# Performance work log

Measured on AMD Instinct MI355X. Metric: run time of the kernel, lower is better.

The kernel has to match this reference:

```python
import jax, jax.numpy as jnp
import numpy as np

B, L, LC, C, CTX, H = 4, 2048, 512, 1024, 1024, 16
D = C // H
EPS = 1e-6
SCALE = 1.0 / np.float32(np.sqrt(D))


def _ln(x):
    # LayerNorm32, elementwise_affine applied outside when present
    mu = jnp.mean(x, axis=-1, keepdims=True)
    var = jnp.var(x, axis=-1, keepdims=True)
    return (x - mu) * jax.lax.rsqrt(var + EPS)


def _attn(q, k, v):
    # q: [B,Lq,H,D], k/v: [B,Lk,H,D] -> [B,Lq,C]
    s = jnp.einsum('bqhd,bkhd->bhqk', q, k) * SCALE
    p = jax.nn.softmax(s, axis=-1)
    o = jnp.einsum('bhqk,bkhd->bqhd', p, v)
    return o.reshape(o.shape[0], o.shape[1], C)


def setup_inputs() -> dict:
    key = jax.random.key(0)
    ks = jax.random.split(key, 12)
    s = 0.02
    w = lambda k, shape: (jax.random.normal(k, shape, jnp.float32) * s)
    z = lambda n: jnp.zeros((n,), jnp.float32)
    return {
        'x': jax.random.normal(ks[0], (B, L, C), jnp.float32),
        'mod': jax.random.normal(ks[1], (B, C), jnp.float32),
        'context': jax.random.normal(ks[2], (B, LC, CTX), jnp.float32),
        'w_ada': w(ks[3], (C, 6 * C)), 'b_ada': z(6 * C),
        'w_qkv': w(ks[4], (C, 3 * C)), 'b_qkv': z(3 * C),
        'w_so': w(ks[5], (C, C)), 'b_so': z(C),
        'g_n2': jnp.ones((C,), jnp.float32), 'b_n2': z(C),
        'w_cq': w(ks[6], (C, C)), 'b_cq': z(C),
        'w_ckv': w(ks[7], (CTX, 2 * C)), 'b_ckv': z(2 * C),
        'w_co': w(ks[8], (C, C)), 'b_co': z(C),
        'w_m1': w(ks[9], (C, 4 * C)), 'b_m1': z(4 * C),
        'w_m2': w(ks[10], (4 * C, C)), 'b_m2': z(C),
    }


def reference(x, mod, context, w_ada, b_ada, w_qkv, b_qkv, w_so, b_so,
              g_n2, b_n2, w_cq, b_cq, w_ckv, b_ckv, w_co, b_co,
              w_m1, b_m1, w_m2, b_m2):
    # adaLN modulation: SiLU -> Linear(C, 6C) -> chunk(6)
    ada = jax.nn.silu(mod) @ w_ada + b_ada  # [B, 6C]
    sh_msa, sc_msa, g_msa, sh_mlp, sc_mlp, g_mlp = jnp.split(ada, 6, axis=-1)
    ex = lambda t: t[:, None, :]  # broadcast per-sample over its token run

    # --- MSA branch ---
    h = _ln(x) * (1.0 + ex(sc_msa)) + ex(sh_msa)
    qkv = (h @ w_qkv + b_qkv).reshape(B, L, 3, H, D)
    h = _attn(qkv[:, :, 0], qkv[:, :, 1], qkv[:, :, 2]) @ w_so + b_so
    x = x + h * ex(g_msa)

    # --- MCA branch (norm2 has affine) ---
    h = _ln(x) * g_n2 + b_n2
    q = (h @ w_cq + b_cq).reshape(B, L, H, D)
    kv = (context @ w_ckv + b_ckv).reshape(B, LC, 2, H, D)
    h = _attn(q, kv[:, :, 0], kv[:, :, 1]) @ w_co + b_co
    x = x + h

    # --- FFN branch ---
    h = _ln(x) * (1.0 + ex(sc_mlp)) + ex(sh_mlp)
    h = jax.nn.gelu(h @ w_m1 + b_m1, approximate=False) @ w_m2 + b_m2
    x = x + h * ex(g_mlp)
    return x
```

## Files before the change

### kernel.cpp

```cpp
#include <hip/hip_runtime.h>
#include <cstdint>

typedef __bf16 bf16;
typedef __bf16 bf16x8 __attribute__((ext_vector_type(8)));
typedef __bf16 bf16x4 __attribute__((ext_vector_type(4)));
typedef float  floatx4 __attribute__((ext_vector_type(4)));
typedef unsigned int uint32x4 __attribute__((ext_vector_type(4)));

#define B_  4
#define L_  2048
#define LC_ 512
#define C_  1024
#define H_  16
#define D_  64

typedef const __attribute__((address_space(1))) unsigned int* as1_u32p;
typedef __attribute__((address_space(3))) unsigned int* as3_u32p;

__device__ __forceinline__ void async16(const void* g, void* l) {
  __builtin_amdgcn_global_load_lds((as1_u32p)g, (as3_u32p)l, 16, 0, 0);
}

__device__ __forceinline__ floatx4 mfma16(bf16x8 a, bf16x8 b, floatx4 c) {
  return __builtin_amdgcn_mfma_f32_16x16x32_bf16(a, b, c, 0, 0, 0);
}

__device__ __forceinline__ bool dt_bf16(const unsigned* dt) { return dt[0] == 0x3F803F80u; }

__device__ __forceinline__ float rd(const void* p, size_t i, bool bf) {
  return bf ? (float)((const bf16*)p)[i] : ((const float*)p)[i];
}

__global__ __launch_bounds__(256) void k_cvt(const void* __restrict__ src, bf16* __restrict__ dst,
                                             int N, const unsigned* __restrict__ dt) {
  bool bf = dt_bf16(dt);
  int i = (blockIdx.x * 256 + threadIdx.x) * 4;
  if (i + 3 < N) {
    for (int j = 0; j < 4; ++j) dst[i + j] = (bf16)rd(src, i + j, bf);
  } else {
    for (int j = 0; j < 4 && i + j < N; ++j) dst[i + j] = (bf16)rd(src, i + j, bf);
  }
}

struct CvtSrcs { const void* s[9]; };
__global__ __launch_bounds__(256) void k_cvt_all(CvtSrcs c, bf16* __restrict__ dst,
                                                 const unsigned* __restrict__ dt) {
  bool bf = dt_bf16(dt);
  int i = blockIdx.x * 256 + threadIdx.x;
  if (i >= 15360) return;
  const int pre[10] = {0, 3072, 4096, 5120, 6144, 7168, 9216, 10240, 14336, 15360};
  int seg = 0;
  #pragma unroll
  for (int k = 1; k < 9; ++k) if (i >= pre[k]) seg = k;
  dst[i] = (bf16)rd(c.s[seg], i - pre[seg], bf);
}

__global__ __launch_bounds__(256) void k_silu(const void* __restrict__ mod, float* __restrict__ sm,
                                              const unsigned* __restrict__ dt) {
  bool bf = dt_bf16(dt);
  int i = blockIdx.x * 256 + threadIdx.x;
  if (i < B_ * C_) {
    float v = rd(mod, i, bf);
    sm[i] = v / (1.f + __expf(-v));
  }
}

__global__ __launch_bounds__(256) void k_ada(const float* __restrict__ sm, const void* __restrict__ w,
                                             float* __restrict__ part, const unsigned* __restrict__ dt) {
  bool bf = dt_bf16(dt);
  int idx = blockIdx.x * 256 + threadIdx.x;
  int b = idx / 6144, j = idx - b * 6144;
  int k0 = blockIdx.y * 256;
  const float* s = sm + b * C_;
  float acc = 0.f;
  if (bf) {
    const bf16* W = (const bf16*)w;
    for (int k = k0; k < k0 + 256; ++k) acc += s[k] * (float)W[(size_t)k * 6144 + j];
  } else {
    const float* W = (const float*)w;
    for (int k = k0; k < k0 + 256; ++k) acc += s[k] * W[(size_t)k * 6144 + j];
  }
  part[(size_t)blockIdx.y * 24576 + idx] = acc;
}

__global__ __launch_bounds__(256) void k_ada_red(const float* __restrict__ part, const void* __restrict__ bv,
                                                 float* __restrict__ ada, const unsigned* __restrict__ dt) {
  bool bf = dt_bf16(dt);
  int idx = blockIdx.x * 256 + threadIdx.x;
  int j = idx % 6144;
  ada[idx] = rd(bv, j, bf) + part[idx] + part[24576 + idx] + part[49152 + idx] + part[73728 + idx];
}

struct TransDesc { const void* src; bf16* dst; int R, Cc, nCb, pre; };
struct TransDescs { TransDesc d[7]; };
__global__ __launch_bounds__(256) void k_trans_all(TransDescs t, const unsigned* __restrict__ dt) {
  bool bf = dt_bf16(dt);
  __shared__ bf16 tile[32][33];
  int blk = blockIdx.x;
  int di = 0;
  #pragma unroll
  for (int i = 1; i < 7; ++i) if (blk >= t.d[i].pre) di = i;
  const void* src = t.d[di].src;
  bf16* dst = t.d[di].dst;
  int R = t.d[di].R, Cc = t.d[di].Cc;
  int local = blk - t.d[di].pre;
  int bx = local % t.d[di].nCb, by = local / t.d[di].nCb;
  int c0 = bx * 32, r0 = by * 32;
  int tx = threadIdx.x & 31, ty = threadIdx.x >> 5;
  for (int i = 0; i < 4; ++i)
    tile[ty * 4 + i][tx] = (bf16)rd(src, (size_t)(r0 + ty * 4 + i) * Cc + c0 + tx, bf);
  __syncthreads();
  for (int i = 0; i < 4; ++i)
    dst[(size_t)(c0 + ty * 4 + i) * R + r0 + tx] = tile[tx][ty * 4 + i];
}

__global__ __launch_bounds__(256) void k_vt(const bf16* __restrict__ src, int ld, int off, int Lk,
                                            bf16* __restrict__ VT) {
  __shared__ bf16 tile[32][33];
  int l0 = blockIdx.x * 32;
  int d0 = blockIdx.y * 32;
  int bh = blockIdx.z, b = bh >> 4, h = bh & 15;
  int tx = threadIdx.x & 31, ty = threadIdx.x >> 5;
  for (int i = 0; i < 4; ++i) {
    int l = l0 + ty * 4 + i;
    tile[ty * 4 + i][tx] = src[((size_t)b * Lk + l) * ld + off + h * 64 + d0 + tx];
  }
  __syncthreads();
  for (int i = 0; i < 4; ++i) {
    int d = d0 + ty * 4 + i;
    VT[((size_t)bh * 64 + d) * Lk + l0 + tx] = tile[tx][ty * 4 + i];
  }
}

__global__ __launch_bounds__(256) void k_ln(const void* __restrict__ xraw, const float* __restrict__ xf,
                                            const unsigned* __restrict__ dt, bf16* __restrict__ out,
                                            const float* __restrict__ ada, int scOff, int shOff, float scAdd,
                                            const bf16* __restrict__ gcol, const bf16* __restrict__ bcol) {
  int row = blockIdx.x;
  int b = row >> 11;
  int base = row * C_ + threadIdx.x * 4;
  float v[4];
  if (xf) {
    for (int i = 0; i < 4; ++i) v[i] = xf[base + i];
  } else {
    bool bf = dt_bf16(dt);
    for (int i = 0; i < 4; ++i) v[i] = rd(xraw, base + i, bf);
  }
  float s1 = 0.f, s2 = 0.f;
  for (int i = 0; i < 4; ++i) { s1 += v[i]; s2 += v[i] * v[i]; }
  for (int m = 1; m < 64; m <<= 1) { s1 += __shfl_xor(s1, m); s2 += __shfl_xor(s2, m); }
  __shared__ float r1[4], r2[4];
  int w = threadIdx.x >> 6;
  if ((threadIdx.x & 63) == 0) { r1[w] = s1; r2[w] = s2; }
  __syncthreads();
  s1 = r1[0] + r1[1] + r1[2] + r1[3];
  s2 = r2[0] + r2[1] + r2[2] + r2[3];
  float mu = s1 * (1.f / (float)C_);
  float var = fmaxf(s2 * (1.f / (float)C_) - mu * mu, 0.f);
  float rstd = rsqrtf(var + 1e-6f);
  for (int i = 0; i < 4; ++i) {
    int c = threadIdx.x * 4 + i;
    float sc, sh;
    if (ada) { sc = scAdd + ada[b * 6144 + scOff + c]; sh = ada[b * 6144 + shOff + c]; }
    else     { sc = (float)gcol[c];                    sh = (float)bcol[c]; }
    out[base + i] = (bf16)((v[i] - mu) * rstd * sc + sh);
  }
}

template <int MODE>
__global__ __launch_bounds__(256) void k_gemm(const bf16* __restrict__ A, const bf16* __restrict__ Bt,
                                              const bf16* __restrict__ bias, void* __restrict__ outv,
                                              int M, int N, int K,
                                              const void* __restrict__ resid,
                                              const float* __restrict__ ada, int gateOff,
                                              const unsigned* __restrict__ dt,
                                              float qs, int qN) {
  __shared__ bf16 As[2 * 8192];
  __shared__ bf16 Bs[2 * 8192];
  const int tid = threadIdx.x;
  const int w = tid >> 6, lane = tid & 63;
  const int wr = w & 1, wc = w >> 1;
  const int g = lane >> 4, t = lane & 15;

  const int nbx = gridDim.x;
  const int nwg = nbx * gridDim.y;
  const int orig = blockIdx.y * nbx + blockIdx.x;
  const int qq = nwg >> 3, rrm = nwg & 7;
  const int xcd = orig & 7, sidx = orig >> 3;
  const int wgid = (xcd < rrm ? xcd * (qq + 1) : rrm * (qq + 1) + (xcd - rrm) * qq) + sidx;
  const int rowA0 = (wgid / nbx) * 128, rowB0 = (wgid % nbx) * 128;

  const int scol = ((lane & 3) ^ ((lane >> 3) & 3)) * 8;
  const bf16* Ag = A  + (size_t)(rowA0 + w * 32 + (lane >> 2)) * K + scol;
  const bf16* Bg = Bt + (size_t)(rowB0 + w * 32 + (lane >> 2)) * K + scol;

  auto stage = [&](int kb, int bufsel) {
    bf16* Ad = As + bufsel * 8192 + w * 1024;
    bf16* Bd = Bs + bufsel * 8192 + w * 1024;
    async16(Ag + kb,                       Ad);
    async16(Ag + kb + (size_t)16 * K,      Ad + 512);
    async16(Ag + kb + 32,                  Ad + 4096);
    async16(Ag + kb + 32 + (size_t)16 * K, Ad + 4096 + 512);
    async16(Bg + kb,                       Bd);
    async16(Bg + kb + (size_t)16 * K,      Bd + 512);
    async16(Bg + kb + 32,                  Bd + 4096);
    async16(Bg + kb + 32 + (size_t)16 * K, Bd + 4096 + 512);
  };

  floatx4 acc[4][4];
  for (int i = 0; i < 4; ++i) for (int j = 0; j < 4; ++j) for (int r = 0; r < 4; ++r) acc[i][j][r] = 0.f;

  stage(0, 0);
  __syncthreads();

  const int rsw = (t >> 1) & 3;

  const int nkb = K >> 6;
  for (int it = 0; it < nkb; ++it) {
    const int cur = it & 1;
    if (it + 1 < nkb) stage((it + 1) << 6, cur ^ 1);
    const bf16* Asb = As + cur * 8192;
    const bf16* Bsb = Bs + cur * 8192;
    __builtin_amdgcn_s_setprio(1);
    #pragma unroll
    for (int kk = 0; kk < 2; ++kk) {
      const int gc = (g ^ rsw) * 8;
      bf16x8 af[4], bfr[4];
      #pragma unroll
      for (int mt = 0; mt < 4; ++mt) af[mt]  = *(const bf16x8*)&Asb[kk * 4096 + (wr * 64 + mt * 16 + t) * 32 + gc];
      #pragma unroll
      for (int nt = 0; nt < 4; ++nt) bfr[nt] = *(const bf16x8*)&Bsb[kk * 4096 + (wc * 64 + nt * 16 + t) * 32 + gc];
      #pragma unroll
      for (int mt = 0; mt < 4; ++mt)
        #pragma unroll
        for (int nt = 0; nt < 4; ++nt)
          acc[mt][nt] = mfma16(af[mt], bfr[nt], acc[mt][nt]);
    }
    __builtin_amdgcn_s_setprio(0);
    if (it + 1 < nkb) __syncthreads();
  }

  const bool bf = (MODE == 1 || MODE == 4) ? dt_bf16(dt) : false;
  for (int mt = 0; mt < 4; ++mt) {
    for (int nt = 0; nt < 4; ++nt) {
      int grow = rowA0 + wr * 64 + mt * 16 + g * 4;
      int gcol = rowB0 + wc * 64 + nt * 16 + t;
      float bvv = (float)bias[gcol];
      for (int r = 0; r < 4; ++r) {
        int rr = grow + r;
        float v = acc[mt][nt][r] + bvv;
        size_t idx = (size_t)rr * N + gcol;
        if (MODE == 0) {
          ((bf16*)outv)[idx] = (bf16)(v * ((gcol < qN) ? qs : 1.0f));
        } else if (MODE == 1) {
          float gt = ada[(rr >> 11) * 6144 + gateOff + gcol];
          ((float*)outv)[idx] = rd(resid, idx, bf) + v * gt;
        } else if (MODE == 2) {
          ((float*)outv)[idx] = ((const float*)resid)[idx] + v;
        } else if (MODE == 3) {
          ((bf16*)outv)[idx] = (bf16)(0.5f * v * (1.f + erff(v * 0.70710678118654752f)));
        } else {
          float gt = ada[(rr >> 11) * 6144 + gateOff + gcol];
          float val = ((const float*)resid)[idx] + v * gt;
          if (bf) ((bf16*)outv)[idx] = (bf16)val;
          else    ((float*)outv)[idx] = val;
        }
      }
    }
  }
}

template <int MODE>
__global__ __launch_bounds__(512) void k_gemm8(const bf16* __restrict__ A, const bf16* __restrict__ Bt,
                                               const bf16* __restrict__ bias, void* __restrict__ outv,
                                               int M, int N, int K,
                                               const void* __restrict__ resid,
                                               const float* __restrict__ ada, int gateOff,
                                               const unsigned* __restrict__ dt,
                                               float qs, int qN) {
  __shared__ bf16 As[2 * 16384];
  __shared__ bf16 Bs[2 * 16384];
  const int tid = threadIdx.x;
  const int lane = tid & 63;
  const int wid = tid >> 6;
  const int wrw = wid & 1, wcw = wid >> 1;
  const int g = lane >> 4, t = lane & 15;

  const int nbx = gridDim.x;
  const int nwg = nbx * gridDim.y;
  const int orig = blockIdx.y * nbx + blockIdx.x;
  const int qq = nwg >> 3, rrm = nwg & 7;
  const int xcd = orig & 7, sidx = orig >> 3;
  const int wgid = (xcd < rrm ? xcd * (qq + 1) : rrm * (qq + 1) + (xcd - rrm) * qq) + sidx;
  const int rowA0 = (wgid / nbx) * 256, rowB0 = (wgid % nbx) * 256;

  const int srow = tid >> 3;
  const int sch = ((tid & 7) ^ (srow & 7)) * 8;
  const bf16* Ag = A  + (size_t)(rowA0 + srow) * K + sch;
  const bf16* Bg = Bt + (size_t)(rowB0 + srow) * K + sch;
  const size_t rstep = (size_t)64 * K;

  floatx4 acc[8][4];
  #pragma unroll
  for (int i = 0; i < 8; ++i)
    #pragma unroll
    for (int j = 0; j < 4; ++j)
      for (int r = 0; r < 4; ++r) acc[i][j][r] = 0.f;

  const int nkb = K >> 6;
  #pragma unroll
  for (int j = 0; j < 4; ++j) async16(Ag + (size_t)j * rstep, As + j * 4096 + tid * 8);
  #pragma unroll
  for (int j = 0; j < 4; ++j) async16(Bg + (size_t)j * rstep, Bs + j * 4096 + tid * 8);

  const int t7 = t & 7;

  for (int T = 0; T < nkb; ++T) {
    const int cur = T & 1;
    const bool st = (T + 1 < nkb);
    const int kb1 = (T + 1) << 6;
    bf16* Asn = As + (cur ^ 1) * 16384;
    bf16* Bsn = Bs + (cur ^ 1) * 16384;

    if (st) {
      async16(Ag + kb1,         Asn + tid * 8);
      async16(Ag + rstep + kb1, Asn + 4096 + tid * 8);
      asm volatile("s_waitcnt vmcnt(2)" ::: "memory");
    } else {
      asm volatile("s_waitcnt vmcnt(0)" ::: "memory");
    }
    __builtin_amdgcn_s_barrier();

    const bf16* Ac = As + cur * 16384;
    const bf16* Bc = Bs + cur * 16384;

    bf16x8 bfr[4];
    #pragma unroll
    for (int nf = 0; nf < 4; ++nf)
      bfr[nf] = *(const bf16x8*)&Bc[(wcw * 64 + nf * 16 + t) * 64 + ((0 * 4 + g) ^ t7) * 8];
    {
      bf16x8 af[4];
      #pragma unroll
      for (int mf = 0; mf < 4; ++mf)
        af[mf] = *(const bf16x8*)&Ac[(wrw * 128 + mf * 16 + t) * 64 + ((0 * 4 + g) ^ t7) * 8];
      __builtin_amdgcn_s_setprio(1);
      #pragma unroll
      for (int mf = 0; mf < 4; ++mf)
        #pragma unroll
        for (int nf = 0; nf < 4; ++nf)
          acc[mf][nf] = mfma16(af[mf], bfr[nf], acc[mf][nf]);
      __builtin_amdgcn_s_setprio(0);
    }
    if (st) {
      async16(Ag + 2 * rstep + kb1, Asn + 2 * 4096 + tid * 8);
      async16(Ag + 3 * rstep + kb1, Asn + 3 * 4096 + tid * 8);
    }
    {
      bf16x8 af[4];
      #pragma unroll
      for (int mf = 0; mf < 4; ++mf)
        af[mf] = *(const bf16x8*)&Ac[(wrw * 128 + (mf + 4) * 16 + t) * 64 + ((0 * 4 + g) ^ t7) * 8];
      __builtin_amdgcn_s_setprio(1);
      #pragma unroll
      for (int mf = 0; mf < 4; ++mf)
        #pragma unroll
        for (int nf = 0; nf < 4; ++nf)
          acc[mf + 4][nf] = mfma16(af[mf], bfr[nf], acc[mf + 4][nf]);
      __builtin_amdgcn_s_setprio(0);
    }
    if (st) {
      async16(Bg + kb1,         Bsn + tid * 8);
      async16(Bg + rstep + kb1, Bsn + 4096 + tid * 8);
    }
    #pragma unroll
    for (int nf = 0; nf < 4; ++nf)
      bfr[nf] = *(const bf16x8*)&Bc[(wcw * 64 + nf * 16 + t) * 64 + ((1 * 4 + g) ^ t7) * 8];
    {
      bf16x8 af[4];
      #pragma unroll
      for (int mf = 0; mf < 4; ++mf)
        af[mf] = *(const bf16x8*)&Ac[(wrw * 128 + mf * 16 + t) * 64 + ((1 * 4 + g) ^ t7) * 8];
      __builtin_amdgcn_s_setprio(1);
      #pragma unroll
      for (int mf = 0; mf < 4; ++mf)
        #pragma unroll
        for (int nf = 0; nf < 4; ++nf)
          acc[mf][nf] = mfma16(af[mf], bfr[nf], acc[mf][nf]);
      __builtin_amdgcn_s_setprio(0);
    }
    if (st) {
      async16(Bg + 2 * rstep + kb1, Bsn + 2 * 4096 + tid * 8);
      async16(Bg + 3 * rstep + kb1, Bsn + 3 * 4096 + tid * 8);
    }
    {
      bf16x8 af[4];
      #pragma unroll
      for (int mf = 0; mf < 4; ++mf)
        af[mf] = *(const bf16x8*)&Ac[(wrw * 128 + (mf + 4) * 16 + t) * 64 + ((1 * 4 + g) ^ t7) * 8];
      __builtin_amdgcn_s_setprio(1);
      #pragma unroll
      for (int mf = 0; mf < 4; ++mf)
        #pragma unroll
        for (int nf = 0; nf < 4; ++nf)
          acc[mf + 4][nf] = mfma16(af[mf], bfr[nf], acc[mf + 4][nf]);
      __builtin_amdgcn_s_setprio(0);
    }
    asm volatile("s_waitcnt lgkmcnt(0)" ::: "memory");
    __builtin_amdgcn_s_barrier();
  }

  const bool bf = (MODE == 1 || MODE == 4) ? dt_bf16(dt) : false;
  #pragma unroll
  for (int mf = 0; mf < 8; ++mf) {
    #pragma unroll
    for (int nf = 0; nf < 4; ++nf) {
      int grow = rowA0 + wrw * 128 + mf * 16 + g * 4;
      int gcol = rowB0 + wcw * 64 + nf * 16 + t;
      float bvv = (float)bias[gcol];
      for (int r = 0; r < 4; ++r) {
        int rr = grow + r;
        float v = acc[mf][nf][r] + bvv;
        size_t idx = (size_t)rr * N + gcol;
        if (MODE == 0) {
          ((bf16*)outv)[idx] = (bf16)(v * ((gcol < qN) ? qs : 1.0f));
        } else if (MODE == 1) {
          float gt = ada[(rr >> 11) * 6144 + gateOff + gcol];
          ((float*)outv)[idx] = rd(resid, idx, bf) + v * gt;
        } else if (MODE == 2) {
          ((float*)outv)[idx] = ((const float*)resid)[idx] + v;
        } else if (MODE == 3) {
          ((bf16*)outv)[idx] = (bf16)(0.5f * v * (1.f + erff(v * 0.70710678118654752f)));
        } else {
          float gt = ada[(rr >> 11) * 6144 + gateOff + gcol];
          float val = ((const float*)resid)[idx] + v * gt;
          if (bf) ((bf16*)outv)[idx] = (bf16)val;
          else    ((float*)outv)[idx] = val;
        }
      }
    }
  }
}

__global__ __launch_bounds__(512) void k_attn(const bf16* __restrict__ Qb, int ldq, int qoff,
                                              const bf16* __restrict__ Kb, int ldk, int koff,
                                              const bf16* __restrict__ VT,
                                              bf16* __restrict__ Ob, int Lk) {
  __shared__ bf16 smem[24576];

  const int tid = threadIdx.x;
  const int w = tid >> 6, lane = tid & 63;
  const int g = lane >> 4, t = lane & 15;
  const int bh = blockIdx.y, b = bh >> 4, h = bh & 15;
  const int q0 = blockIdx.x * 128;

  const bf16* Q  = Qb + (size_t)(b * L_ + q0) * ldq + h * 64 + qoff;
  const bf16* K  = Kb + (size_t)b * Lk * ldk + h * 64 + koff;
  const bf16* Vt = VT + (size_t)bh * 64 * Lk;
  const int rowQ = w * 16 + t;
  bf16* O = Ob + ((size_t)(b * L_ + q0 + rowQ)) * C_ + h * 64;

  const int sp  = lane & 7;
  const int sq0 = w * 16 + (lane >> 3);
  const int sq1 = sq0 + 8;
  const int swq0 = (sp ^ (sq0 & 7)) * 8;
  const int swq1 = (sp ^ (sq1 & 7)) * 8;
  const int skr = w * 8 + (lane >> 3);
  const int swk = (sp ^ (skr & 7)) * 8;

  bf16* Ps  = smem;
  bf16* KB0 = smem + 8192;
  bf16* VB0 = smem + 16384;

  async16(Q + (size_t)sq0 * ldq + swq0, smem + w * 1024);
  async16(Q + (size_t)sq1 * ldq + swq1, smem + w * 1024 + 512);
  async16(K + (size_t)skr * ldk + swk, KB0 + w * 512);
  async16(Vt + (size_t)skr * Lk + swk, VB0 + w * 512);
  __syncthreads();

  bf16x8 bq[2];
  #pragma unroll
  for (int ko = 0; ko < 2; ++ko)
    bq[ko] = *(const bf16x8*)&smem[rowQ * 64 + (((ko * 4 + g) ^ (rowQ & 7)) * 8)];

  const int nt = Lk >> 6;

  if (nt > 1) {
    async16(K + (size_t)(64 + skr) * ldk + swk, KB0 + 4096 + w * 512);
  }

  floatx4 s[4];
  __builtin_amdgcn_s_setprio(1);
  #pragma unroll
  for (int mt = 0; mt < 4; ++mt) {
    floatx4 sa; for (int r = 0; r < 4; ++r) sa[r] = 0.f;
    #pragma unroll
    for (int ko = 0; ko < 2; ++ko) {
      int rowK = mt * 16 + t;
      bf16x8 ak = *(const bf16x8*)&KB0[rowK * 64 + (((ko * 4 + g) ^ (rowK & 7)) * 8)];
      sa = mfma16(ak, bq[ko], sa);
    }
    s[mt] = sa;
  }
  __builtin_amdgcn_s_setprio(0);
  __syncthreads();

  bf16x8 ones;
  #pragma unroll
  for (int i = 0; i < 8; ++i) ones[i] = (bf16)1.0f;

  floatx4 o_acc[4], o_sum;
  for (int d = 0; d < 4; ++d) for (int r = 0; r < 4; ++r) o_acc[d][r] = 0.f;
  for (int r = 0; r < 4; ++r) o_sum[r] = 0.f;

  const size_t kstep = (size_t)64 * ldk;
  const bf16* Kst = K + (size_t)(128 + skr) * ldk + swk;
  const bf16* Vst = Vt + (size_t)skr * Lk + 64 + swk;

  for (int ti = 0; ti < nt; ++ti) {
    const int cur = ti & 1;

    if (ti + 2 < nt) {
      async16(Kst, KB0 + cur * 4096 + w * 512);
    }
    if (ti + 1 < nt) {
      async16(Vst, VB0 + ((ti + 1) & 1) * 4096 + w * 512);
    }
    Kst += kstep; Vst += 64;

    float sv[16];
    #pragma unroll
    for (int mt = 0; mt < 4; ++mt)
      #pragma unroll
      for (int r = 0; r < 4; ++r) sv[mt * 4 + r] = exp2f(s[mt][r]);

    #pragma unroll
    for (int mt = 0; mt < 4; ++mt) {
      bf16x4 pk;
      for (int r = 0; r < 4; ++r) pk[r] = (bf16)sv[mt * 4 + r];
      int off = mt * 16 + g * 4;
      int chunk = off >> 3, sub = off & 7;
      *(bf16x4*)&Ps[rowQ * 64 + ((chunk ^ (rowQ & 7)) * 8) + sub] = pk;
    }

    if (ti + 1 < nt) {
      const bf16* Kc = KB0 + ((ti + 1) & 1) * 4096;
      __builtin_amdgcn_s_setprio(1);
      #pragma unroll
      for (int mt = 0; mt < 4; ++mt) {
        floatx4 sa; for (int r = 0; r < 4; ++r) sa[r] = 0.f;
        #pragma unroll
        for (int ko = 0; ko < 2; ++ko) {
          int rowK = mt * 16 + t;
          bf16x8 ak = *(const bf16x8*)&Kc[rowK * 64 + (((ko * 4 + g) ^ (rowK & 7)) * 8)];
          sa = mfma16(ak, bq[ko], sa);
        }
        s[mt] = sa;
      }
      __builtin_amdgcn_s_setprio(0);
    }

    const bf16* Vc = VB0 + cur * 4096;
    __builtin_amdgcn_s_setprio(1);
    #pragma unroll
    for (int ko = 0; ko < 2; ++ko) {
      bf16x8 bp = *(const bf16x8*)&Ps[rowQ * 64 + (((ko * 4 + g) ^ (rowQ & 7)) * 8)];
      o_sum = mfma16(ones, bp, o_sum);
      #pragma unroll
      for (int d = 0; d < 4; ++d) {
        int rowV = d * 16 + t;
        bf16x8 av = *(const bf16x8*)&Vc[rowV * 64 + (((ko * 4 + g) ^ (rowV & 7)) * 8)];
        o_acc[d] = mfma16(av, bp, o_acc[d]);
      }
    }
    __builtin_amdgcn_s_setprio(0);

    if (ti + 1 < nt) __syncthreads();
  }

  float rl = 1.f / o_sum[0];
  #pragma unroll
  for (int d = 0; d < 4; ++d) {
    bf16x4 ov;
    for (int r = 0; r < 4; ++r) ov[r] = (bf16)(o_acc[d][r] * rl);
    *(bf16x4*)&O[d * 16 + g * 4] = ov;
  }
}

extern "C" void kernel_launch(void* const* d_in, const int* in_sizes, int n_in,
                              void* d_out, int out_size, void* d_ws, size_t ws_size,
                              hipStream_t stream) {
  const void* x     = d_in[0];
  const void* mod   = d_in[1];
  const void* ctx   = d_in[2];
  const void* w_ada = d_in[3];
  const void* b_ada = d_in[4];
  const void* w_qkv = d_in[5];
  const void* b_qkv = d_in[6];
  const void* w_so  = d_in[7];
  const void* b_so  = d_in[8];
  const void* g_n2  = d_in[9];
  const void* b_n2  = d_in[10];
  const void* w_cq  = d_in[11];
  const void* b_cq  = d_in[12];
  const void* w_ckv = d_in[13];
  const void* b_ckv = d_in[14];
  const void* w_co  = d_in[15];
  const void* b_co  = d_in[16];
  const void* w_m1  = d_in[17];
  const void* b_m1  = d_in[18];
  const void* w_m2  = d_in[19];
  const void* b_m2  = d_in[20];
  const unsigned* dt = (const unsigned*)g_n2;

  char* p = (char*)d_ws;
  auto alloc = [&](size_t bytes) { char* r = p; p += (bytes + 255) & ~(size_t)255; return r; };
  float* sm    = (float*)alloc((size_t)B_ * C_ * 4);
  float* adp   = (float*)alloc((size_t)4 * 24576 * 4);
  float* ada   = (float*)alloc((size_t)B_ * 6144 * 4);
  bf16* wT_qkv = (bf16*)alloc((size_t)3072 * 1024 * 2);
  bf16* wT_so  = (bf16*)alloc((size_t)1024 * 1024 * 2);
  bf16* wT_cq  = (bf16*)alloc((size_t)1024 * 1024 * 2);
  bf16* wT_ckv = (bf16*)alloc((size_t)2048 * 1024 * 2);
  bf16* wT_co  = (bf16*)alloc((size_t)1024 * 1024 * 2);
  bf16* wT_m1  = (bf16*)alloc((size_t)4096 * 1024 * 2);
  bf16* wT_m2  = (bf16*)alloc((size_t)1024 * 4096 * 2);
  bf16* hb     = (bf16*)alloc((size_t)8192 * 1024 * 2);
  bf16* qkvb   = (bf16*)alloc((size_t)8192 * 3072 * 2);
  bf16* attn_o = (bf16*)alloc((size_t)8192 * 1024 * 2);
  float* xcur  = (float*)alloc((size_t)8192 * 1024 * 4);
  bf16* ctxb   = (bf16*)alloc((size_t)B_ * LC_ * 1024 * 2);
  bf16* biasb  = (bf16*)alloc(15360 * 2);
  bf16* bqkvb = biasb;
  bf16* bsob  = biasb + 3072;
  bf16* g2b   = biasb + 4096;
  bf16* b2b   = biasb + 5120;
  bf16* bcqb  = biasb + 6144;
  bf16* bckvb = biasb + 7168;
  bf16* bcob  = biasb + 9216;
  bf16* bm1b  = biasb + 10240;
  bf16* bm2b  = biasb + 14336;
  bf16* q2   = qkvb;
  bf16* kv   = qkvb + (size_t)8192 * 1024;
  bf16* gbuf = qkvb;
  bf16* vt   = hb;
  if (ws_size < (size_t)(p - (char*)d_ws)) return;

  dim3 blk(256);
  dim3 blkA(512);
  k_silu<<<16, blk, 0, stream>>>(mod, sm, dt);
  k_ada<<<dim3(96, 4), blk, 0, stream>>>(sm, w_ada, adp, dt);
  k_ada_red<<<96, blk, 0, stream>>>(adp, b_ada, ada, dt);
  k_cvt<<<2048, blk, 0, stream>>>(ctx, ctxb, B_ * LC_ * 1024, dt);
  CvtSrcs cs = {{b_qkv, b_so, g_n2, b_n2, b_cq, b_ckv, b_co, b_m1, b_m2}};
  k_cvt_all<<<60, blk, 0, stream>>>(cs, biasb, dt);
  TransDescs td = {{
    {w_qkv, wT_qkv, 1024, 3072,  96, 0},
    {w_so,  wT_so,  1024, 1024,  32, 3072},
    {w_cq,  wT_cq,  1024, 1024,  32, 4096},
    {w_ckv, wT_ckv, 1024, 2048,  64, 5120},
    {w_co,  wT_co,  1024, 1024,  32, 7168},
    {w_m1,  wT_m1,  1024, 4096, 128, 8192},
    {w_m2,  wT_m2,  4096, 1024,  32, 12288},
  }};
  k_trans_all<<<16384, blk, 0, stream>>>(td, dt);

  const float SC_L2E = 0.125f * 1.44269504088896f;

  k_ln<<<8192, blk, 0, stream>>>(x, nullptr, dt, hb, ada, 1024, 0, 1.0f, nullptr, nullptr);
  k_gemm<0><<<dim3(24, 64), blk, 0, stream>>>(hb, wT_qkv, bqkvb, qkvb, 8192, 3072, 1024, nullptr, nullptr, 0, dt, SC_L2E, 1024);
  k_vt<<<dim3(64, 2, 64), blk, 0, stream>>>(qkvb, 3072, 2048, L_, vt);
  k_attn<<<dim3(16, 64), blkA, 0, stream>>>(qkvb, 3072, 0, qkvb, 3072, 1024, vt, attn_o, L_);
  k_gemm<1><<<dim3(8, 64), blk, 0, stream>>>(attn_o, wT_so, bsob, xcur, 8192, 1024, 1024, x, ada, 2048, dt, 1.f, 0);

  k_ln<<<8192, blk, 0, stream>>>(nullptr, xcur, dt, hb, nullptr, 0, 0, 0.f, g2b, b2b);
  k_gemm<0><<<dim3(8, 64), blk, 0, stream>>>(hb, wT_cq, bcqb, q2, 8192, 1024, 1024, nullptr, nullptr, 0, dt, SC_L2E, 1024);
  k_gemm<0><<<dim3(16, 16), blk, 0, stream>>>(ctxb, wT_ckv, bckvb, kv, 2048, 2048, 1024, nullptr, nullptr, 0, dt, 1.f, 0);
  k_vt<<<dim3(16, 2, 64), blk, 0, stream>>>(kv, 2048, 1024, LC_, vt);
  k_attn<<<dim3(16, 64), blkA, 0, stream>>>(q2, 1024, 0, kv, 2048, 0, vt, attn_o, LC_);
  k_gemm<2><<<dim3(8, 64), blk, 0, stream>>>(attn_o, wT_co, bcob, xcur, 8192, 1024, 1024, xcur, nullptr, 0, dt, 1.f, 0);

  k_ln<<<8192, blk, 0, stream>>>(nullptr, xcur, dt, hb, ada, 4096, 3072, 1.0f, nullptr, nullptr);
  k_gemm8<3><<<dim3(16, 32), blkA, 0, stream>>>(hb, wT_m1, bm1b, gbuf, 8192, 4096, 1024, nullptr, nullptr, 0, dt, 1.f, 0);
  k_gemm<4><<<dim3(8, 64), blk, 0, stream>>>(gbuf, wT_m2, bm2b, d_out, 8192, 1024, 4096, xcur, ada, 5120, dt, 1.f, 0);
}
```

Baseline: 815.7 us.

## Add 512-thread 256x128 GEMM variant for N=1024 projections

Adds a new GEMM kernel with 8 waves per 512-thread block computing a 256x128 output tile (each wave 64x64), double-buffered LDS with async global-to-LDS loads and an XCD-aware workgroup remap. The N=1024 GEMMs (self-attn out, cross q, cross out, MLP down) switch from the 256-thread kernel to this one with half as many blocks. The aim is more B-tile reuse per block and better latency hiding from more waves. In exchange it uses more LDS per block, which may reduce occupancy, and leaves fewer blocks to fill the GPU.

```diff
diff --git a/kernel.cpp b/kernel.cpp
--- a/kernel.cpp
+++ b/kernel.cpp
@@ -415,6 +415,144 @@
     #pragma unroll
     for (int nf = 0; nf < 4; ++nf) {
       int grow = rowA0 + wrw * 128 + mf * 16 + g * 4;
+      int gcol = rowB0 + wcw * 64 + nf * 16 + t;
+      float bvv = (float)bias[gcol];
+      for (int r = 0; r < 4; ++r) {
+        int rr = grow + r;
+        float v = acc[mf][nf][r] + bvv;
+        size_t idx = (size_t)rr * N + gcol;
+        if (MODE == 0) {
+          ((bf16*)outv)[idx] = (bf16)(v * ((gcol < qN) ? qs : 1.0f));
+        } else if (MODE == 1) {
+          float gt = ada[(rr >> 11) * 6144 + gateOff + gcol];
+          ((float*)outv)[idx] = rd(resid, idx, bf) + v * gt;
+        } else if (MODE == 2) {
+          ((float*)outv)[idx] = ((const float*)resid)[idx] + v;
+        } else if (MODE == 3) {
+          ((bf16*)outv)[idx] = (bf16)(0.5f * v * (1.f + erff(v * 0.70710678118654752f)));
+        } else {
+          float gt = ada[(rr >> 11) * 6144 + gateOff + gcol];
+          float val = ((const float*)resid)[idx] + v * gt;
+          if (bf) ((bf16*)outv)[idx] = (bf16)val;
+          else    ((float*)outv)[idx] = val;
+        }
+      }
+    }
+  }
+}
+
+template <int MODE>
+__global__ __launch_bounds__(512) void k_gemm8n(const bf16* __restrict__ A, const bf16* __restrict__ Bt,
+                                                const bf16* __restrict__ bias, void* __restrict__ outv,
+                                                int M, int N, int K,
+                                                const void* __restrict__ resid,
+                                                const float* __restrict__ ada, int gateOff,
+                                                const unsigned* __restrict__ dt,
+                                                float qs, int qN) {
+  __shared__ bf16 As[2 * 16384];
+  __shared__ bf16 Bs[2 * 8192];
+  const int tid = threadIdx.x;
+  const int lane = tid & 63;
+  const int wid = tid >> 6;
+  const int wrw = wid & 3, wcw = wid >> 2;
+  const int g = lane >> 4, t = lane & 15;
+
+  const int nbx = gridDim.x;
+  const int nwg = nbx * gridDim.y;
+  const int orig = blockIdx.y * nbx + blockIdx.x;
+  const int qq = nwg >> 3, rrm = nwg & 7;
+  const int xcd = orig & 7, sidx = orig >> 3;
+  const int wgid = (xcd < rrm ? xcd * (qq + 1) : rrm * (qq + 1) + (xcd - rrm) * qq) + sidx;
+  const int rowA0 = (wgid / nbx) * 256, rowB0 = (wgid % nbx) * 128;
+
+  const int srow = tid >> 3;
+  const int sch = ((tid & 7) ^ (srow & 7)) * 8;
+  const bf16* Ag = A  + (size_t)(rowA0 + srow) * K + sch;
+  const bf16* Bg = Bt + (size_t)(rowB0 + srow) * K + sch;
+  const size_t rstep = (size_t)64 * K;
+
+  floatx4 acc[4][4];
+  #pragma unroll
+  for (int i = 0; i < 4; ++i)
+    #pragma unroll
+    for (int j = 0; j < 4; ++j)
+      for (int r = 0; r < 4; ++r) acc[i][j][r] = 0.f;
+
+  const int nkb = K >> 6;
+  #pragma unroll
+  for (int j = 0; j < 4; ++j) async16(Ag + (size_t)j * rstep, As + j * 4096 + tid * 8);
+  #pragma unroll
+  for (int j = 0; j < 2; ++j) async16(Bg + (size_t)j * rstep, Bs + j * 4096 + tid * 8);
+
+  const int t7 = t & 7;
+
+  for (int T = 0; T < nkb; ++T) {
+    const int cur = T & 1;
+    const bool st = (T + 1 < nkb);
+    const int kb1 = (T + 1) << 6;
+    bf16* Asn = As + (cur ^ 1) * 16384;
+    bf16* Bsn = Bs + (cur ^ 1) * 8192;
+
+    if (st) {
+      async16(Ag + kb1,         Asn + tid * 8);
+      async16(Ag + rstep + kb1, Asn + 4096 + tid * 8);
+      asm volatile("s_waitcnt vmcnt(2)" ::: "memory");
+    } else {
+      asm volatile("s_waitcnt vmcnt(0)" ::: "memory");
+    }
+    __builtin_amdgcn_s_barrier();
+
+    const bf16* Ac = As + cur * 16384;
+    const bf16* Bc = Bs + cur * 8192;
+
+    {
+      bf16x8 af[4], bfr[4];
+      #pragma unroll
+      for (int nf = 0; nf < 4; ++nf)
+        bfr[nf] = *(const bf16x8*)&Bc[(wcw * 64 + nf * 16 + t) * 64 + ((0 * 4 + g) ^ t7) * 8];
+      #pragma unroll
+      for (int mf = 0; mf < 4; ++mf)
+        af[mf] = *(const bf16x8*)&Ac[(wrw * 64 + mf * 16 + t) * 64 + ((0 * 4 + g) ^ t7) * 8];
+      __builtin_amdgcn_s_setprio(1);
+      #pragma unroll
+      for (int mf = 0; mf < 4; ++mf)
+        #pragma unroll
+        for (int nf = 0; nf < 4; ++nf)
+          acc[mf][nf] = mfma16(af[mf], bfr[nf], acc[mf][nf]);
+      __builtin_amdgcn_s_setprio(0);
+    }
+    if (st) {
+      async16(Ag + 2 * rstep + kb1, Asn + 2 * 4096 + tid * 8);
+      async16(Ag + 3 * rstep + kb1, Asn + 3 * 4096 + tid * 8);
+      async16(Bg + kb1,             Bsn + tid * 8);
+      async16(Bg + rstep + kb1,     Bsn + 4096 + tid * 8);
+    }
+    {
+      bf16x8 af[4], bfr[4];
+      #pragma unroll
+      for (int nf = 0; nf < 4; ++nf)
+        bfr[nf] = *(const bf16x8*)&Bc[(wcw * 64 + nf * 16 + t) * 64 + ((1 * 4 + g) ^ t7) * 8];
+      #pragma unroll
+      for (int mf = 0; mf < 4; ++mf)
+        af[mf] = *(const bf16x8*)&Ac[(wrw * 64 + mf * 16 + t) * 64 + ((1 * 4 + g) ^ t7) * 8];
+      __builtin_amdgcn_s_setprio(1);
+      #pragma unroll
+      for (int mf = 0; mf < 4; ++mf)
+        #pragma unroll
+        for (int nf = 0; nf < 4; ++nf)
+          acc[mf][nf] = mfma16(af[mf], bfr[nf], acc[mf][nf]);
+      __builtin_amdgcn_s_setprio(0);
+    }
+    asm volatile("s_waitcnt lgkmcnt(0)" ::: "memory");
+    __builtin_amdgcn_s_barrier();
+  }
+
+  const bool bf = (MODE == 1 || MODE == 4) ? dt_bf16(dt) : false;
+  #pragma unroll
+  for (int mf = 0; mf < 4; ++mf) {
+    #pragma unroll
+    for (int nf = 0; nf < 4; ++nf) {
+      int grow = rowA0 + wrw * 64 + mf * 16 + g * 4;
       int gcol = rowB0 + wcw * 64 + nf * 16 + t;
       float bvv = (float)bias[gcol];
       for (int r = 0; r < 4; ++r) {
@@ -670,16 +808,16 @@
   k_gemm<0><<<dim3(24, 64), blk, 0, stream>>>(hb, wT_qkv, bqkvb, qkvb, 8192, 3072, 1024, nullptr, nullptr, 0, dt, SC_L2E, 1024);
   k_vt<<<dim3(64, 2, 64), blk, 0, stream>>>(qkvb, 3072, 2048, L_, vt);
   k_attn<<<dim3(16, 64), blkA, 0, stream>>>(qkvb, 3072, 0, qkvb, 3072, 1024, vt, attn_o, L_);
-  k_gemm<1><<<dim3(8, 64), blk, 0, stream>>>(attn_o, wT_so, bsob, xcur, 8192, 1024, 1024, x, ada, 2048, dt, 1.f, 0);
+  k_gemm8n<1><<<dim3(8, 32), blkA, 0, stream>>>(attn_o, wT_so, bsob, xcur, 8192, 1024, 1024, x, ada, 2048, dt, 1.f, 0);
 
   k_ln<<<8192, blk, 0, stream>>>(nullptr, xcur, dt, hb, nullptr, 0, 0, 0.f, g2b, b2b);
-  k_gemm<0><<<dim3(8, 64), blk, 0, stream>>>(hb, wT_cq, bcqb, q2, 8192, 1024, 1024, nullptr, nullptr, 0, dt, SC_L2E, 1024);
+  k_gemm8n<0><<<dim3(8, 32), blkA, 0, stream>>>(hb, wT_cq, bcqb, q2, 8192, 1024, 1024, nullptr, nullptr, 0, dt, SC_L2E, 1024);
   k_gemm<0><<<dim3(16, 16), blk, 0, stream>>>(ctxb, wT_ckv, bckvb, kv, 2048, 2048, 1024, nullptr, nullptr, 0, dt, 1.f, 0);
   k_vt<<<dim3(16, 2, 64), blk, 0, stream>>>(kv, 2048, 1024, LC_, vt);
   k_attn<<<dim3(16, 64), blkA, 0, stream>>>(q2, 1024, 0, kv, 2048, 0, vt, attn_o, LC_);
-  k_gemm<2><<<dim3(8, 64), blk, 0, stream>>>(attn_o, wT_co, bcob, xcur, 8192, 1024, 1024, xcur, nullptr, 0, dt, 1.f, 0);
+  k_gemm8n<2><<<dim3(8, 32), blkA, 0, stream>>>(attn_o, wT_co, bcob, xcur, 8192, 1024, 1024, xcur, nullptr, 0, dt, 1.f, 0);
 
   k_ln<<<8192, blk, 0, stream>>>(nullptr, xcur, dt, hb, ada, 4096, 3072, 1.0f, nullptr, nullptr);
   k_gemm8<3><<<dim3(16, 32), blkA, 0, stream>>>(hb, wT_m1, bm1b, gbuf, 8192, 4096, 1024, nullptr, nullptr, 0, dt, 1.f, 0);
-  k_gemm<4><<<dim3(8, 64), blk, 0, stream>>>(gbuf, wT_m2, bm2b, d_out, 8192, 1024, 4096, xcur, ada, 5120, dt, 1.f, 0);
-}
+  k_gemm8n<4><<<dim3(8, 32), blkA, 0, stream>>>(gbuf, wT_m2, bm2b, d_out, 8192, 1024, 4096, xcur, ada, 5120, dt, 1.f, 0);
+}
```

Result: slower. 851.4 us (+4.4%).
